# Kernel tuning notes

Hardware: AMD Instinct MI355X
Metric: run time of the kernel (lower is better)

## Reference

```python
import jax, jax.numpy as jnp
import numpy as np

B, T, D, H, DK, DV, W, CHUNK = 2, 4096, 2048, 8, 128, 256, 4, 64
EPS_NORM = 1e-5
EPS_L2 = 1e-6


def silu(x):
    return x * jax.nn.sigmoid(x)


def causal_dwconv(x, w):
    # x: [B, T, C], w: [C, W]; torch Conv1d (cross-correlation) with left pad W-1,
    # keeping the first T outputs => strictly causal depthwise conv.
    Wk = w.shape[1]
    Tlen = x.shape[1]
    xp = jnp.pad(x, ((0, 0), (Wk - 1, 0), (0, 0)))
    return sum(xp[:, i:i + Tlen, :] * w[:, i] for i in range(Wk))


def l2norm(x):
    return x * jax.lax.rsqrt(jnp.sum(x * x, axis=-1, keepdims=True) + EPS_L2)


def delta_chunk(S, inp):
    # Gated delta-rule recurrence over one chunk. S: [B,H,DK,DV]
    # S_t = exp(g_t) * S_{t-1}; err = v_t - k_t^T S_t; S_t += k_t (beta_t * err)^T; o_t = q_t^T S_t
    def step(S, t):
        q_t, k_t, v_t, g_t, b_t = t
        S = S * jnp.exp(g_t)[..., None, None]
        err = v_t - jnp.einsum('bhk,bhkv->bhv', k_t, S)
        S = S + k_t[..., :, None] * (b_t[..., None] * err)[..., None, :]
        o_t = jnp.einsum('bhk,bhkv->bhv', q_t, S)
        return S, o_t
    return jax.lax.scan(step, S, inp)


def reference(x, Wq, Wk, Wv, Wb, Wa, Wg, Wo, conv_q, conv_k, conv_v, A_log, dt_bias, g_norm_w):
    # short causal depthwise conv + silu on q/k/v projections
    q = silu(causal_dwconv(x @ Wq, conv_q))
    k = silu(causal_dwconv(x @ Wk, conv_k))
    v = silu(causal_dwconv(x @ Wv, conv_v))
    beta = jax.nn.sigmoid(x @ Wb)                              # [B,T,H]
    g = -jnp.exp(A_log) * jax.nn.softplus(x @ Wa + dt_bias)   # [B,T,H], log-decay <= 0
    q = l2norm(q.reshape(B, T, H, DK)) * (DK ** -0.5)
    k = l2norm(k.reshape(B, T, H, DK))
    v = v.reshape(B, T, H, DV)

    def to_chunks(a):  # [B,T,...] -> [T//CHUNK, CHUNK, B, ...]
        return a.swapaxes(0, 1).reshape(T // CHUNK, CHUNK, a.shape[0], *a.shape[2:])

    inp = (to_chunks(q), to_chunks(k), to_chunks(v), to_chunks(g), to_chunks(beta))
    S0 = jnp.zeros((B, H, DK, DV), x.dtype)
    _, o = jax.lax.scan(jax.checkpoint(delta_chunk), S0, inp)  # o: [Nc,CHUNK,B,H,DV]
    o = o.reshape(T, B, H, DV).swapaxes(0, 1)                  # [B,T,H,DV]

    # per-head gated RMSNorm (FusedRMSNormGated with silu gate) then output projection
    gate = (x @ Wg).reshape(B, T, H, DV)
    o = o * jax.lax.rsqrt(jnp.mean(o * o, axis=-1, keepdims=True) + EPS_NORM)
    o = o * g_norm_w * silu(gate)
    return o.reshape(B, T, H * DV) @ Wo


def setup_inputs() -> dict:
    key = jax.random.key(0)
    ks = jax.random.split(key, 14)
    s = 0.02
    f = jnp.float32
    x = jax.random.normal(ks[0], (B, T, D), f)
    Wq = jax.random.normal(ks[1], (D, H * DK), f) * s
    Wk = jax.random.normal(ks[2], (D, H * DK), f) * s
    Wv = jax.random.normal(ks[3], (D, H * DV), f) * s
    Wb = jax.random.normal(ks[4], (D, H), f) * s
    Wa = jax.random.normal(ks[5], (D, H), f) * s
    Wg = jax.random.normal(ks[6], (D, H * DV), f) * s
    Wo = jax.random.normal(ks[7], (H * DV, D), f) * s
    conv_q = jax.random.normal(ks[8], (H * DK, W), f) * 0.2
    conv_k = jax.random.normal(ks[9], (H * DK, W), f) * 0.2
    conv_v = jax.random.normal(ks[10], (H * DV, W), f) * 0.2
    A_log = jnp.log(jax.random.uniform(ks[11], (H,), f, 1.0, 16.0))
    dt_bias = jax.random.normal(ks[12], (H,), f) * 0.5
    g_norm_w = jnp.ones((DV,), f)
    return dict(x=x, Wq=Wq, Wk=Wk, Wv=Wv, Wb=Wb, Wa=Wa, Wg=Wg, Wo=Wo,
                conv_q=conv_q, conv_k=conv_k, conv_v=conv_v,
                A_log=A_log, dt_bias=dt_bias, g_norm_w=g_norm_w)
```

## Files before the change

### kernel.cpp

```cpp
#include <hip/hip_runtime.h>
#include <cstdint>
#include <cstddef>

#define B_ 2
#define T_ 4096
#define D_ 2048
#define H_ 8
#define DK_ 128
#define DV_ 256
#define BT_ (B_*T_)
#define NQK_ 1024
#define NV_ 2048
#define N1_ 6144

typedef __bf16 bf16x8 __attribute__((ext_vector_type(8)));
typedef float f32x4 __attribute__((ext_vector_type(4)));

#define GAS __attribute__((address_space(1)))
#define LAS __attribute__((address_space(3)))

__device__ __forceinline__ float bfu(unsigned short u) {
  union { unsigned int i; float f; } c; c.i = ((unsigned int)u) << 16; return c.f;
}
__device__ __forceinline__ float bflo(unsigned int u) {
  union { unsigned int i; float f; } c; c.i = u << 16; return c.f;
}
__device__ __forceinline__ float bfhi(unsigned int u) {
  union { unsigned int i; float f; } c; c.i = u & 0xFFFF0000u; return c.f;
}
__device__ __forceinline__ unsigned short f2bf(float f) {
  union { float f; unsigned int i; } c; c.f = f;
  unsigned int x = c.i;
  x += 0x7FFFu + ((x >> 16) & 1u);
  return (unsigned short)(x >> 16);
}
__device__ __forceinline__ unsigned int pack2(float a, float b) {
  return (unsigned int)f2bf(a) | ((unsigned int)f2bf(b) << 16);
}
__device__ __forceinline__ float siluf(float x) { return x / (1.f + __expf(-x)); }
__device__ __forceinline__ float redsum32(float v) {
  #pragma unroll
  for (int m = 16; m >= 1; m >>= 1) v += __shfl_xor(v, m);
  return v;
}
__device__ __forceinline__ void async_copy16(void* lds, const void* gsrc) {
  __builtin_amdgcn_global_load_lds((const GAS unsigned int*)gsrc,
                                   (LAS unsigned int*)lds, 16, 0, 0);
}

template<int CTRL>
__device__ __forceinline__ float dpp_add(float x) {
  union { int i; float f; } a, r;
  a.f = x;
  r.i = __builtin_amdgcn_update_dpp(0, a.i, CTRL, 0xF, 0xF, true);
  return x + r.f;
}
__device__ __forceinline__ float red16_ror(float x) {
  x = dpp_add<0x121>(x);
  x = dpp_add<0x122>(x);
  x = dpp_add<0x124>(x);
  x = dpp_add<0x128>(x);
  return x;
}

__global__ __launch_bounds__(256) void cast_x_kernel(const float* __restrict__ in,
                                                     unsigned short* __restrict__ out) {
  size_t i = ((size_t)blockIdx.x * 256 + threadIdx.x) * 4;
  float4 v = *(const float4*)(in + i);
  uint2 r;
  r.x = pack2(v.x, v.y);
  r.y = pack2(v.z, v.w);
  *(uint2*)(out + i) = r;
}

__global__ __launch_bounds__(256) void transpose_cast(const float* __restrict__ in,
                                                      unsigned short* __restrict__ out,
                                                      int R, int Cc) {
  __shared__ float tile[32][33];
  int c0 = blockIdx.x * 32, r0 = blockIdx.y * 32;
  int tx = threadIdx.x, ty = threadIdx.y;
  #pragma unroll
  for (int i = 0; i < 4; ++i)
    tile[ty + i*8][tx] = in[(size_t)(r0 + ty + i*8) * Cc + c0 + tx];
  __syncthreads();
  #pragma unroll
  for (int i = 0; i < 4; ++i)
    out[(size_t)(c0 + ty + i*8) * R + r0 + tx] = f2bf(tile[tx][ty + i*8]);
}

template<int BF16OUT>
__global__ __launch_bounds__(256) void gemm_kernel(
    const unsigned short* __restrict__ A,
    const unsigned short* __restrict__ Bt,
    void* __restrict__ Cout,
    int M, int N, int K)
{
  __shared__ __align__(16) unsigned short As[128][32];
  __shared__ __align__(16) unsigned short Bs[128][32];
  const int tid  = threadIdx.x;
  const int lane = tid & 63;
  const int wave = tid >> 6;
  const int wr = wave >> 1, wc = wave & 1;
  const int row0 = blockIdx.y * 128, col0 = blockIdx.x * 128;
  f32x4 acc[4][4];
  #pragma unroll
  for (int m = 0; m < 4; ++m)
    #pragma unroll
    for (int n = 0; n < 4; ++n)
      acc[m][n] = (f32x4){0.f, 0.f, 0.f, 0.f};

  const int fr = lane & 15;
  const int fq = lane >> 4;

  for (int k0 = 0; k0 < K; k0 += 32) {
    #pragma unroll
    for (int i = 0; i < 2; ++i) {
      int c = tid + i * 256;
      int r = c >> 2, o = (c & 3) * 8;
      async_copy16(&As[r][o], A  + (size_t)(row0 + r) * K + k0 + o);
      async_copy16(&Bs[r][o], Bt + (size_t)(col0 + r) * K + k0 + o);
    }
    asm volatile("s_waitcnt vmcnt(0)" ::: "memory");
    __syncthreads();
    bf16x8 af[4], bfr[4];
    #pragma unroll
    for (int m = 0; m < 4; ++m)
      af[m] = *(const bf16x8*)&As[wr*64 + m*16 + fr][fq*8];
    #pragma unroll
    for (int n = 0; n < 4; ++n)
      bfr[n] = *(const bf16x8*)&Bs[wc*64 + n*16 + fr][fq*8];
    #pragma unroll
    for (int m = 0; m < 4; ++m)
      #pragma unroll
      for (int n = 0; n < 4; ++n)
        acc[m][n] = __builtin_amdgcn_mfma_f32_16x16x32_bf16(af[m], bfr[n], acc[m][n], 0, 0, 0);
    __syncthreads();
  }
  const int fc = lane & 15, fg = lane >> 4;
  #pragma unroll
  for (int m = 0; m < 4; ++m)
    #pragma unroll
    for (int n = 0; n < 4; ++n)
      #pragma unroll
      for (int r = 0; r < 4; ++r) {
        size_t idx = (size_t)(row0 + wr*64 + m*16 + fg*4 + r) * N
                   + (col0 + wc*64 + n*16 + fc);
        if (BF16OUT) ((unsigned short*)Cout)[idx] = f2bf(acc[m][n][r]);
        else         ((float*)Cout)[idx]          = acc[m][n][r];
      }
}

__global__ __launch_bounds__(256) void beta_g_kernel(
    const float* __restrict__ x, const float* __restrict__ Wb, const float* __restrict__ Wa,
    const float* __restrict__ A_log, const float* __restrict__ dtb,
    float* __restrict__ bg)
{
  const int t = blockIdx.x;
  const int wave = threadIdx.x >> 6;
  const int lane = threadIdx.x & 63;
  const float* xr = x + (size_t)t * D_;
  float acc[4] = {0.f, 0.f, 0.f, 0.f};
  for (int k = lane; k < D_; k += 64) {
    float xv = xr[k];
    #pragma unroll
    for (int i = 0; i < 4; ++i) {
      int o = wave + 4 * i;
      float w = (o < 8) ? Wb[(size_t)k * 8 + o] : Wa[(size_t)k * 8 + (o - 8)];
      acc[i] += xv * w;
    }
  }
  #pragma unroll
  for (int i = 0; i < 4; ++i) {
    #pragma unroll
    for (int m = 32; m >= 1; m >>= 1) acc[i] += __shfl_xor(acc[i], m);
  }
  if (lane == 0) {
    #pragma unroll
    for (int i = 0; i < 4; ++i) {
      int o = wave + 4 * i;
      if (o < 8) {
        bg[((size_t)t * H_ + o) * 2] = 1.f / (1.f + __expf(-acc[i]));
      } else {
        int h = o - 8;
        float z = acc[i] + dtb[h];
        float sp = (z > 20.f) ? z : log1pf(__expf(z));
        bg[((size_t)t * H_ + h) * 2 + 1] = __expf(-__expf(A_log[h]) * sp);
      }
    }
  }
}

__global__ __launch_bounds__(256) void conv_kernel(
    const unsigned short* __restrict__ Y1,
    const float* __restrict__ cq, const float* __restrict__ ck, const float* __restrict__ cv,
    float* __restrict__ qf, float* __restrict__ kf, float* __restrict__ vf)
{
  const int t  = blockIdx.x;
  const int tt = t & (T_ - 1);
  const int tid = threadIdx.x;
  const int c4 = tid * 4;
  const int c8 = tid * 8;

  float wqa[4][4], wka[4][4], wva[8][4];
  #pragma unroll
  for (int m = 0; m < 4; ++m) {
    float4 a = *(const float4*)(cq + (size_t)(c4 + m) * 4);
    wqa[m][0] = a.x; wqa[m][1] = a.y; wqa[m][2] = a.z; wqa[m][3] = a.w;
    float4 b = *(const float4*)(ck + (size_t)(c4 + m) * 4);
    wka[m][0] = b.x; wka[m][1] = b.y; wka[m][2] = b.z; wka[m][3] = b.w;
  }
  #pragma unroll
  for (int m = 0; m < 8; ++m) {
    float4 a = *(const float4*)(cv + (size_t)(c8 + m) * 4);
    wva[m][0] = a.x; wva[m][1] = a.y; wva[m][2] = a.z; wva[m][3] = a.w;
  }

  float aq[4] = {0,0,0,0}, ak[4] = {0,0,0,0}, av[8] = {0,0,0,0,0,0,0,0};
  #pragma unroll
  for (int i = 0; i < 4; ++i) {
    if (tt + i >= 3) {
      const unsigned short* row = Y1 + (size_t)(t + i - 3) * N1_;
      ushort4 yq = *(const ushort4*)(row + c4);
      ushort4 yk = *(const ushort4*)(row + NQK_ + c4);
      int4    yv = *(const int4*)(row + 2 * NQK_ + c8);
      float qv[4] = { bfu(yq.x), bfu(yq.y), bfu(yq.z), bfu(yq.w) };
      float kv[4] = { bfu(yk.x), bfu(yk.y), bfu(yk.z), bfu(yk.w) };
      unsigned int vu[4] = { (unsigned)yv.x, (unsigned)yv.y, (unsigned)yv.z, (unsigned)yv.w };
      float vv[8] = { bflo(vu[0]), bfhi(vu[0]), bflo(vu[1]), bfhi(vu[1]),
                      bflo(vu[2]), bfhi(vu[2]), bflo(vu[3]), bfhi(vu[3]) };
      #pragma unroll
      for (int m = 0; m < 4; ++m) { aq[m] += qv[m] * wqa[m][i]; ak[m] += kv[m] * wka[m][i]; }
      #pragma unroll
      for (int m = 0; m < 8; ++m) av[m] += vv[m] * wva[m][i];
    }
  }
  float sq[4], sk[4], ssq = 0.f, ssk = 0.f;
  #pragma unroll
  for (int m = 0; m < 4; ++m) {
    sq[m] = siluf(aq[m]); ssq += sq[m] * sq[m];
    sk[m] = siluf(ak[m]); ssk += sk[m] * sk[m];
  }
  ssq = redsum32(ssq);
  ssk = redsum32(ssk);
  float scq = rsqrtf(ssq + 1e-6f) * 0.08838834764831845f;
  float sck = rsqrtf(ssk + 1e-6f);
  float4 oq = { sq[0]*scq, sq[1]*scq, sq[2]*scq, sq[3]*scq };
  float4 ok = { sk[0]*sck, sk[1]*sck, sk[2]*sck, sk[3]*sck };
  *(float4*)(qf + (size_t)t * NQK_ + c4) = oq;
  *(float4*)(kf + (size_t)t * NQK_ + c4) = ok;
  float4 ov0 = { siluf(av[0]), siluf(av[1]), siluf(av[2]), siluf(av[3]) };
  float4 ov1 = { siluf(av[4]), siluf(av[5]), siluf(av[6]), siluf(av[7]) };
  *(float4*)(vf + (size_t)t * NV_ + c8)     = ov0;
  *(float4*)(vf + (size_t)t * NV_ + c8 + 4) = ov1;
}

__global__ __launch_bounds__(64, 1) void delta_kernel(
    const float* __restrict__ qf, const float* __restrict__ kf,
    const float* __restrict__ vf, const float* __restrict__ bg,
    float* __restrict__ o)
{
  const int blk = blockIdx.x;
  const int bh = blk & 15;
  const int jq = blk >> 4;
  const int b = bh >> 3, h = bh & 7;
  const int lane = threadIdx.x;
  const int r = lane & 15;
  const int j = jq * 4 + (lane >> 4);

  const int SQK = H_ * DK_;
  const int SV  = H_ * DV_;

  const float* qp = qf + (size_t)(b * T_) * SQK + h * DK_ + r * 8;
  const float* kp = kf + (size_t)(b * T_) * SQK + h * DK_ + r * 8;
  const float* vp = vf + (size_t)(b * T_) * SV + h * DV_ + j;
  const float* gp = bg + ((size_t)(b * T_) * H_ + h) * 2;
  float*       op = o  + (size_t)(b * T_) * SV + h * DV_ + j;

  float4 Sa = {0,0,0,0}, Sb = {0,0,0,0};

  float4 ka0,kb0,qa0,qb0, ka1,kb1,qa1,qb1, ka2,kb2,qa2,qb2, ka3,kb3,qa3,qb3,
         ka4,kb4,qa4,qb4, ka5,kb5,qa5,qb5, ka6,kb6,qa6,qb6, ka7,kb7,qa7,qb7;
  float  vv0,vv1,vv2,vv3,vv4,vv5,vv6,vv7;
  float2 bgv0,bgv1,bgv2,bgv3,bgv4,bgv5,bgv6,bgv7;

#define PREF(SL, ROW) do { \
    ka##SL = *(const float4*)(kp + (ROW) * SQK); \
    kb##SL = *(const float4*)(kp + (ROW) * SQK + 4); \
    qa##SL = *(const float4*)(qp + (ROW) * SQK); \
    qb##SL = *(const float4*)(qp + (ROW) * SQK + 4); \
    vv##SL = vp[(ROW) * SV]; \
    bgv##SL = *(const float2*)(gp + (ROW) * (H_ * 2)); \
    __builtin_amdgcn_sched_barrier(0); \
  } while (0)

#define STEP(SL) do { \
    float p0 = ka##SL.x*Sa.x, p1 = ka##SL.y*Sa.y, p2 = ka##SL.z*Sa.z, p3 = ka##SL.w*Sa.w; \
    float p4 = kb##SL.x*Sb.x, p5 = kb##SL.y*Sb.y, p6 = kb##SL.z*Sb.z, p7 = kb##SL.w*Sb.w; \
    float part = ((p0 + p1) + (p2 + p3)) + ((p4 + p5) + (p6 + p7)); \
    float dot = red16_ror(part); \
    float gm = bgv##SL.y; \
    float u = bgv##SL.x * fmaf(-gm, dot, vv##SL); \
    Sa.x = fmaf(gm, Sa.x, ka##SL.x * u); \
    Sa.y = fmaf(gm, Sa.y, ka##SL.y * u); \
    Sa.z = fmaf(gm, Sa.z, ka##SL.z * u); \
    Sa.w = fmaf(gm, Sa.w, ka##SL.w * u); \
    Sb.x = fmaf(gm, Sb.x, kb##SL.x * u); \
    Sb.y = fmaf(gm, Sb.y, kb##SL.y * u); \
    Sb.z = fmaf(gm, Sb.z, kb##SL.z * u); \
    Sb.w = fmaf(gm, Sb.w, kb##SL.w * u); \
    float o0 = qa##SL.x*Sa.x, o1 = qa##SL.y*Sa.y, o2 = qa##SL.z*Sa.z, o3 = qa##SL.w*Sa.w; \
    float o4 = qb##SL.x*Sb.x, o5 = qb##SL.y*Sb.y, o6 = qb##SL.z*Sb.z, o7 = qb##SL.w*Sb.w; \
    float pov = ((o0 + o1) + (o2 + o3)) + ((o4 + o5) + (o6 + o7)); \
    float od = red16_ror(pov); \
    if (r == 0) *op = od; \
    op += SV; \
  } while (0)

  PREF(0,0); PREF(1,1); PREF(2,2); PREF(3,3);
  PREF(4,4); PREF(5,5); PREF(6,6); PREF(7,7);
  qp += 8 * SQK; kp += 8 * SQK; vp += 8 * SV; gp += 8 * (H_ * 2);

  for (int t = 0; t < T_; t += 8) {
    STEP(0); PREF(0,0);
    STEP(1); PREF(1,1);
    STEP(2); PREF(2,2);
    STEP(3); PREF(3,3);
    STEP(4); PREF(4,4);
    STEP(5); PREF(5,5);
    STEP(6); PREF(6,6);
    STEP(7); PREF(7,7);
    qp += 8 * SQK; kp += 8 * SQK; vp += 8 * SV; gp += 8 * (H_ * 2);
  }
#undef PREF
#undef STEP
}

__global__ __launch_bounds__(256) void post_kernel(
    const float* __restrict__ o, const unsigned short* __restrict__ Y1,
    const float* __restrict__ gw, unsigned short* __restrict__ og)
{
  const int t = blockIdx.x;
  const int tid = threadIdx.x;
  const int e = tid * 8;
  float4 v0 = *(const float4*)(o + (size_t)t * NV_ + e);
  float4 v1 = *(const float4*)(o + (size_t)t * NV_ + e + 4);
  float v[8] = { v0.x, v0.y, v0.z, v0.w, v1.x, v1.y, v1.z, v1.w };
  float ss = 0.f;
  #pragma unroll
  for (int m = 0; m < 8; ++m) ss += v[m] * v[m];
  ss = redsum32(ss);
  float rms = rsqrtf(ss * (1.f / 256.f) + 1e-5f);
  int4 graw = *(const int4*)(Y1 + (size_t)t * N1_ + 4096 + e);
  unsigned int gu[4] = { (unsigned)graw.x, (unsigned)graw.y, (unsigned)graw.z, (unsigned)graw.w };
  float gv[8] = { bflo(gu[0]), bfhi(gu[0]), bflo(gu[1]), bfhi(gu[1]),
                  bflo(gu[2]), bfhi(gu[2]), bflo(gu[3]), bfhi(gu[3]) };
  const int dv = e & 255;
  float res[8];
  #pragma unroll
  for (int m = 0; m < 8; ++m) res[m] = v[m] * rms * gw[dv + m] * siluf(gv[m]);
  int4 outv;
  outv.x = (int)pack2(res[0], res[1]);
  outv.y = (int)pack2(res[2], res[3]);
  outv.z = (int)pack2(res[4], res[5]);
  outv.w = (int)pack2(res[6], res[7]);
  *(int4*)(og + (size_t)t * NV_ + e) = outv;
}

extern "C" void kernel_launch(void* const* d_in, const int* in_sizes, int n_in,
                              void* d_out, int out_size, void* d_ws, size_t ws_size,
                              hipStream_t stream)
{
  (void)in_sizes; (void)n_in; (void)out_size;
  const float* x     = (const float*)d_in[0];
  const float* Wq    = (const float*)d_in[1];
  const float* Wk    = (const float*)d_in[2];
  const float* Wv    = (const float*)d_in[3];
  const float* Wb    = (const float*)d_in[4];
  const float* Wa    = (const float*)d_in[5];
  const float* Wg    = (const float*)d_in[6];
  const float* Wo    = (const float*)d_in[7];
  const float* cq    = (const float*)d_in[8];
  const float* ck    = (const float*)d_in[9];
  const float* cv    = (const float*)d_in[10];
  const float* A_log = (const float*)d_in[11];
  const float* dtb   = (const float*)d_in[12];
  const float* gw    = (const float*)d_in[13];

  char* ws = (char*)d_ws;
  const size_t SZ_XB  = (size_t)BT_ * D_ * 2;
  const size_t SZ_WCT = (size_t)N1_ * D_ * 2;
  const size_t SZ_QF  = (size_t)BT_ * NQK_ * 4;
  const size_t SZ_KF  = (size_t)BT_ * NQK_ * 4;
  const size_t SZ_VF  = (size_t)BT_ * NV_ * 4;
  const size_t SZ_R1a = SZ_XB + SZ_WCT;
  const size_t SZ_R1b = SZ_QF + SZ_KF + SZ_VF;
  const size_t SZ_R1  = (SZ_R1a > SZ_R1b) ? SZ_R1a : SZ_R1b;
  const size_t SZ_WOT = (size_t)D_ * D_ * 2;
  const size_t SZ_BG  = (size_t)BT_ * H_ * 8;
  const size_t SZ_Y1  = (size_t)BT_ * N1_ * 2;

  const size_t OFF_WOT = SZ_R1;
  const size_t OFF_BG  = OFF_WOT + SZ_WOT;
  const size_t OFF_Y1  = OFF_BG + SZ_BG;
  const size_t WS_NEEDED = OFF_Y1 + SZ_Y1;
  if (ws_size < WS_NEEDED) return;

  unsigned short* xb  = (unsigned short*)(ws);
  unsigned short* Wct = (unsigned short*)(ws + SZ_XB);
  float* qf = (float*)(ws);
  float* kf = (float*)(ws + SZ_QF);
  float* vf = (float*)(ws + SZ_QF + SZ_KF);
  float* ov = vf;
  unsigned short* og  = (unsigned short*)(ws);
  unsigned short* Wot = (unsigned short*)(ws + OFF_WOT);
  float* bg   = (float*)(ws + OFF_BG);
  unsigned short* Y1  = (unsigned short*)(ws + OFF_Y1);

  cast_x_kernel<<<(BT_ * D_) / 1024, 256, 0, stream>>>(x, xb);
  dim3 tb(32, 8);
  transpose_cast<<<dim3(1024/32, 2048/32), tb, 0, stream>>>(Wq, Wct, 2048, 1024);
  transpose_cast<<<dim3(1024/32, 2048/32), tb, 0, stream>>>(Wk, Wct + (size_t)1024 * 2048, 2048, 1024);
  transpose_cast<<<dim3(2048/32, 2048/32), tb, 0, stream>>>(Wv, Wct + (size_t)2048 * 2048, 2048, 2048);
  transpose_cast<<<dim3(2048/32, 2048/32), tb, 0, stream>>>(Wg, Wct + (size_t)4096 * 2048, 2048, 2048);
  transpose_cast<<<dim3(2048/32, 2048/32), tb, 0, stream>>>(Wo, Wot, 2048, 2048);

  gemm_kernel<1><<<dim3(N1_/128, BT_/128), 256, 0, stream>>>(xb, Wct, Y1, BT_, N1_, D_);
  beta_g_kernel<<<BT_, 256, 0, stream>>>(x, Wb, Wa, A_log, dtb, bg);
  conv_kernel<<<BT_, 256, 0, stream>>>(Y1, cq, ck, cv, qf, kf, vf);
  delta_kernel<<<B_ * H_ * (DV_/4), 64, 0, stream>>>(qf, kf, vf, bg, ov);
  post_kernel<<<BT_, 256, 0, stream>>>(ov, Y1, gw, og);
  gemm_kernel<0><<<dim3(D_/128, BT_/128), 256, 0, stream>>>(og, Wot, d_out, BT_, D_, D_);
}
```

Before: 1.945 ms.

## Stage v and gate/beta through LDS with async global_load_lds ring buffer

The delta recurrence kernel now stages the per-step v values and beta/decay pairs into an 8-slot LDS ring via global_load_lds, issued seven tiles ahead and paced with a manual vmcnt wait. The q/k register prefetch depth drops from 8 to 2 steps, which frees registers and removes the per-step sched_barrier. The goal is to hide the latency of the scattered scalar v and gate loads on this latency-bound serial scan. The hand-tuned vmcnt(15) count is fragile: if the outstanding-load accounting is off, the kernel can read LDS slots before their data arrives.

```diff
diff --git a/kernel.cpp b/kernel.cpp
--- a/kernel.cpp
+++ b/kernel.cpp
@@ -259,47 +259,62 @@
     const float* __restrict__ vf, const float* __restrict__ bg,
     float* __restrict__ o)
 {
+  __shared__ float vbg_lds[8 * 64];
+
   const int blk = blockIdx.x;
   const int bh = blk & 15;
   const int jq = blk >> 4;
   const int b = bh >> 3, h = bh & 7;
   const int lane = threadIdx.x;
   const int r = lane & 15;
-  const int j = jq * 4 + (lane >> 4);
+  const int g = lane >> 4;
+  const int j0 = jq * 4;
 
   const int SQK = H_ * DK_;
   const int SV  = H_ * DV_;
 
   const float* qp = qf + (size_t)(b * T_) * SQK + h * DK_ + r * 8;
   const float* kp = kf + (size_t)(b * T_) * SQK + h * DK_ + r * 8;
-  const float* vp = vf + (size_t)(b * T_) * SV + h * DV_ + j;
-  const float* gp = bg + ((size_t)(b * T_) * H_ + h) * 2;
-  float*       op = o  + (size_t)(b * T_) * SV + h * DV_ + j;
+  float*       op = o  + (size_t)(b * T_) * SV + h * DV_ + j0 + g;
+
+  const float* stgsrc;
+  int stgstep;
+  if (lane < 32) {
+    stgsrc = vf + ((size_t)(b * T_) + (lane >> 2)) * SV + h * DV_ + j0 + (lane & 3);
+    stgstep = 8 * SV;
+  } else {
+    int l2 = (lane - 32) & 15;
+    stgsrc = bg + ((size_t)(b * T_) + (l2 >> 1)) * (H_ * 2) + h * 2 + (l2 & 1);
+    stgstep = 8 * H_ * 2;
+  }
 
   float4 Sa = {0,0,0,0}, Sb = {0,0,0,0};
-
-  float4 ka0,kb0,qa0,qb0, ka1,kb1,qa1,qb1, ka2,kb2,qa2,qb2, ka3,kb3,qa3,qb3,
-         ka4,kb4,qa4,qb4, ka5,kb5,qa5,qb5, ka6,kb6,qa6,qb6, ka7,kb7,qa7,qb7;
-  float  vv0,vv1,vv2,vv3,vv4,vv5,vv6,vv7;
-  float2 bgv0,bgv1,bgv2,bgv3,bgv4,bgv5,bgv6,bgv7;
-
-#define PREF(SL, ROW) do { \
+  float4 ka0,kb0,qa0,qb0, ka1,kb1,qa1,qb1, ka2,kb2,qa2,qb2, ka3,kb3,qa3,qb3;
+
+#define STAGE(SLOT) do { \
+    __builtin_amdgcn_global_load_lds((const GAS unsigned int*)stgsrc, \
+        (LAS unsigned int*)(vbg_lds + (SLOT) * 64), 4, 0, 0); \
+    stgsrc += stgstep; \
+  } while (0)
+
+#define PREFQK(SL, ROW) do { \
     ka##SL = *(const float4*)(kp + (ROW) * SQK); \
     kb##SL = *(const float4*)(kp + (ROW) * SQK + 4); \
     qa##SL = *(const float4*)(qp + (ROW) * SQK); \
     qb##SL = *(const float4*)(qp + (ROW) * SQK + 4); \
-    vv##SL = vp[(ROW) * SV]; \
-    bgv##SL = *(const float2*)(gp + (ROW) * (H_ * 2)); \
-    __builtin_amdgcn_sched_barrier(0); \
   } while (0)
 
-#define STEP(SL) do { \
+#define FENCE asm volatile("" ::: "memory")
+
+#define STEPX(SL, RT) do { \
+    float vvx = vbg_lds[sofs + (RT) * 4 + g]; \
+    float2 bgv = *(const float2*)&vbg_lds[sofs + 32 + (RT) * 2]; \
     float p0 = ka##SL.x*Sa.x, p1 = ka##SL.y*Sa.y, p2 = ka##SL.z*Sa.z, p3 = ka##SL.w*Sa.w; \
     float p4 = kb##SL.x*Sb.x, p5 = kb##SL.y*Sb.y, p6 = kb##SL.z*Sb.z, p7 = kb##SL.w*Sb.w; \
     float part = ((p0 + p1) + (p2 + p3)) + ((p4 + p5) + (p6 + p7)); \
     float dot = red16_ror(part); \
-    float gm = bgv##SL.y; \
-    float u = bgv##SL.x * fmaf(-gm, dot, vv##SL); \
+    float gm = bgv.y; \
+    float u = bgv.x * fmaf(-gm, dot, vvx); \
     Sa.x = fmaf(gm, Sa.x, ka##SL.x * u); \
     Sa.y = fmaf(gm, Sa.y, ka##SL.y * u); \
     Sa.z = fmaf(gm, Sa.z, ka##SL.z * u); \
@@ -316,23 +331,30 @@
     op += SV; \
   } while (0)
 
-  PREF(0,0); PREF(1,1); PREF(2,2); PREF(3,3);
-  PREF(4,4); PREF(5,5); PREF(6,6); PREF(7,7);
-  qp += 8 * SQK; kp += 8 * SQK; vp += 8 * SV; gp += 8 * (H_ * 2);
-
-  for (int t = 0; t < T_; t += 8) {
-    STEP(0); PREF(0,0);
-    STEP(1); PREF(1,1);
-    STEP(2); PREF(2,2);
-    STEP(3); PREF(3,3);
-    STEP(4); PREF(4,4);
-    STEP(5); PREF(5,5);
-    STEP(6); PREF(6,6);
-    STEP(7); PREF(7,7);
-    qp += 8 * SQK; kp += 8 * SQK; vp += 8 * SV; gp += 8 * (H_ * 2);
-  }
-#undef PREF
-#undef STEP
+  const int NTILES = T_ / 8;
+
+  STAGE(0); STAGE(1); STAGE(2); STAGE(3); STAGE(4); STAGE(5); STAGE(6);
+  PREFQK(0, 0);
+  PREFQK(1, 1);
+
+  for (int c = 0; c < NTILES; ++c) {
+    if (c + 7 < NTILES) STAGE((c + 7) & 7);
+    asm volatile("s_waitcnt vmcnt(15)" ::: "memory");
+    const int sofs = (c & 7) * 64;
+    PREFQK(2, 2); FENCE; STEPX(0, 0);
+    PREFQK(3, 3); FENCE; STEPX(1, 1);
+    PREFQK(0, 4); FENCE; STEPX(2, 2);
+    PREFQK(1, 5); FENCE; STEPX(3, 3);
+    PREFQK(2, 6); FENCE; STEPX(0, 4);
+    PREFQK(3, 7); FENCE; STEPX(1, 5);
+    PREFQK(0, 8); FENCE; STEPX(2, 6);
+    PREFQK(1, 9); FENCE; STEPX(3, 7);
+    qp += 8 * SQK; kp += 8 * SQK;
+  }
+#undef STAGE
+#undef PREFQK
+#undef FENCE
+#undef STEPX
 }
 
 __global__ __launch_bounds__(256) void post_kernel(
```

Result: slower. 2.006 ms (+3.2%).
